# Kernel optimization log

Measured on AMD Instinct MI355X. Metric: run time of the kernel, lower is better.

Reference implementation:

```python
import jax, jax.numpy as jnp
import numpy as np

B, S, D_MODEL, H = 2, 2048, 512, 8
D_HEAD = D_MODEL // H  # 64; d_qk == d_model here


def setup_inputs() -> dict:
    key = jax.random.key(0)
    ks = jax.random.split(key, 7)
    sc = 1.0 / np.sqrt(D_MODEL)
    return {
        "x": jax.random.normal(ks[0], (B, S, D_MODEL), dtype=jnp.float32),
        "Wqk_w": jax.random.normal(ks[1], (2 * D_MODEL, D_MODEL), dtype=jnp.float32) * sc,
        "Wqk_b": jax.random.normal(ks[2], (2 * D_MODEL,), dtype=jnp.float32) * 0.01,
        "Wv_w": jax.random.normal(ks[3], (D_MODEL, D_MODEL), dtype=jnp.float32) * sc,
        "Wv_b": jax.random.normal(ks[4], (D_MODEL,), dtype=jnp.float32) * 0.01,
        "Wo_w": jax.random.normal(ks[5], (D_MODEL, D_MODEL), dtype=jnp.float32) * sc,
        "Wo_b": jax.random.normal(ks[6], (D_MODEL,), dtype=jnp.float32) * 0.01,
    }


def reference(x, Wqk_w, Wqk_b, Wv_w, Wv_b, Wo_w, Wo_b):
    b, s, _ = x.shape
    # projections
    qk = x @ Wqk_w.T + Wqk_b              # [B,S,2*d_qk]
    v = x @ Wv_w.T + Wv_b                 # [B,S,d_model]
    qk = qk.reshape(b, s, 2, H, D_HEAD)   # (two h d) layout
    v = v.reshape(b, s, H, D_HEAD)
    q, k = qk[:, :, 0], qk[:, :, 1]
    # generalized linear attention feature map: elu(x)+1
    q = jax.nn.elu(q) + 1.0
    k = jax.nn.elu(k) + 1.0
    scores = jnp.einsum('bthd,bshd->bhts', q, k)          # [B,H,T,S]
    mask = jnp.tril(jnp.ones((s, s), dtype=scores.dtype))  # causal multiplicative mask
    scores = scores * mask
    nu = scores.sum(axis=-1, keepdims=True)               # row normalizer
    attention = scores / nu
    context = jnp.einsum('bhts,bshd->bthd', attention, v)  # [B,T,H,D]
    out = context.reshape(b, s, D_MODEL) @ Wo_w.T + Wo_b
    return out
```

## Files before the change

kernel.cpp:

```cpp
#include <hip/hip_runtime.h>
#include <math.h>

#define B_N 2
#define S_N 2048
#define DM  512
#define H_N 8
#define DH  64
#define NC  32
#define CH  64

typedef __bf16 bf16x8 __attribute__((ext_vector_type(8)));
typedef float  f32x4  __attribute__((ext_vector_type(4)));

__device__ __forceinline__ unsigned short f2bf(float f) {
    unsigned int u = __float_as_uint(f);
    u += 0x7FFFu + ((u >> 16) & 1u);
    return (unsigned short)(u >> 16);
}
__device__ __forceinline__ float bf2f(unsigned short u) {
    return __uint_as_float((unsigned int)u << 16);
}

__device__ __forceinline__ void gload16(const void* g, void* l) {
    __builtin_amdgcn_global_load_lds(
        (const __attribute__((address_space(1))) unsigned int*)g,
        (__attribute__((address_space(3))) unsigned int*)l, 16, 0, 0);
}

__global__ __launch_bounds__(256) void convert_bf16(
    const float* __restrict__ x,  const float* __restrict__ wqk,
    const float* __restrict__ wv, const float* __restrict__ wo,
    unsigned short* __restrict__ xb,  unsigned short* __restrict__ wqkb,
    unsigned short* __restrict__ wvb, unsigned short* __restrict__ wob)
{
    int gid = blockIdx.x * 256 + threadIdx.x;
    const float* src; unsigned short* dst; int off;
    if (gid < 524288)      { src = x;   dst = xb;   off = gid; }
    else if (gid < 655360) { src = wqk; dst = wqkb; off = gid - 524288; }
    else if (gid < 720896) { src = wv;  dst = wvb;  off = gid - 655360; }
    else                   { src = wo;  dst = wob;  off = gid - 720896; }
    float4 v = ((const float4*)src)[off];
    ushort4 r; r.x = f2bf(v.x); r.y = f2bf(v.y); r.z = f2bf(v.z); r.w = f2bf(v.w);
    ((ushort4*)dst)[off] = r;
}

__global__ __launch_bounds__(256) void gemm_qkv_mfma(
    const unsigned short* __restrict__ xb,
    const unsigned short* __restrict__ Wqkb,
    const unsigned short* __restrict__ Wvb,
    const float* __restrict__ bqk, const float* __restrict__ bv,
    unsigned short* __restrict__ qb, unsigned short* __restrict__ kb_,
    unsigned short* __restrict__ ktb, unsigned short* __restrict__ vtb)
{
    __shared__ unsigned short Alds[128 * 32];
    __shared__ unsigned short Blds[128 * 32];
    const int tid = threadIdx.x;
    const int w = tid >> 6, l = tid & 63;
    const int wm = w >> 1, wn = w & 1;
    const int lane15 = l & 15, quad = l >> 4;
    const int n0 = blockIdx.x * 128;
    const int m0 = blockIdx.y * 128;

    const unsigned short* Wb; const float* bias; int nc0;
    if (n0 < 1024) { Wb = Wqkb; bias = bqk; nc0 = n0;        }
    else           { Wb = Wvb;  bias = bv;  nc0 = n0 - 1024; }

    const int srow = w * 16 + (l >> 2);
    const int skof = (l & 3) << 3;

    f32x4 acc[4][4];
    #pragma unroll
    for (int i = 0; i < 4; i++)
        #pragma unroll
        for (int j = 0; j < 4; j++) acc[i][j] = (f32x4){0.f, 0.f, 0.f, 0.f};

    for (int k0 = 0; k0 < DM; k0 += 32) {
        __syncthreads();
        gload16(&xb[(size_t)(m0 + srow) * DM + k0 + skof],       (char*)Alds + w * 1024);
        gload16(&xb[(size_t)(m0 + 64 + srow) * DM + k0 + skof],  (char*)Alds + 4096 + w * 1024);
        gload16(&Wb[(size_t)(nc0 + srow) * DM + k0 + skof],      (char*)Blds + w * 1024);
        gload16(&Wb[(size_t)(nc0 + 64 + srow) * DM + k0 + skof], (char*)Blds + 4096 + w * 1024);
        __syncthreads();

        bf16x8 af[4], bfr[4];
        #pragma unroll
        for (int i = 0; i < 4; i++) {
            af[i]  = *(bf16x8*)&Alds[(wm * 64 + i * 16 + lane15) * 32 + quad * 8];
            bfr[i] = *(bf16x8*)&Blds[(wn * 64 + i * 16 + lane15) * 32 + quad * 8];
        }
        #pragma unroll
        for (int i = 0; i < 4; i++)
            #pragma unroll
            for (int j = 0; j < 4; j++)
                acc[i][j] = __builtin_amdgcn_mfma_f32_16x16x32_bf16(af[i], bfr[j], acc[i][j], 0, 0, 0);
    }

    #pragma unroll
    for (int i = 0; i < 4; i++) {
        #pragma unroll
        for (int rg = 0; rg < 4; rg++) {
            int m = m0 + wm * 64 + i * 16 + quad * 4 + rg;
            int bb = m >> 11;
            int t  = m & (S_N - 1);
            #pragma unroll
            for (int j = 0; j < 4; j++) {
                int ncol = wn * 64 + j * 16 + lane15;
                float val = acc[i][j][rg] + bias[nc0 + ncol];
                int n = n0 + ncol;
                if (n < 1024) val = (val > 0.f) ? (val + 1.f) : __expf(val);
                unsigned short us = f2bf(val);
                if (n < 512) {
                    int h = n >> 6, d = n & 63;
                    qb[(((size_t)bb * H_N + h) * S_N + t) * DH + d] = us;
                } else if (n < 1024) {
                    int nn = n - 512, h = nn >> 6, d = nn & 63;
                    kb_[(((size_t)bb * H_N + h) * S_N + t) * DH + d] = us;
                    ktb[(((size_t)bb * H_N + h) * DH + d) * S_N + t] = us;
                } else {
                    int nn = n - 1024, h = nn >> 6, d = nn & 63;
                    vtb[(((size_t)bb * H_N + h) * DH + d) * S_N + t] = us;
                }
            }
        }
    }
}

__global__ __launch_bounds__(256) void chunk_sums_mfma(
    const unsigned short* __restrict__ ktb, const unsigned short* __restrict__ vtb,
    float* __restrict__ Asum, float* __restrict__ zsum)
{
    __shared__ float zpart[64][4];
    const int blk = blockIdx.x;
    const int bh = blk >> 5, c = blk & 31;
    const unsigned short* ktc = ktb + (size_t)bh * DH * S_N + c * CH;
    const unsigned short* vtc = vtb + (size_t)bh * DH * S_N + c * CH;
    const int tid = threadIdx.x;
    const int w = tid >> 6, l = tid & 63;
    const int lane15 = l & 15, quad = l >> 4;

    bf16x8 va[2];
    #pragma unroll
    for (int s = 0; s < 2; s++)
        va[s] = *(const bf16x8*)&vtc[(size_t)(w * 16 + lane15) * S_N + s * 32 + quad * 8];

    f32x4 acc[4];
    #pragma unroll
    for (int j = 0; j < 4; j++) acc[j] = (f32x4){0.f, 0.f, 0.f, 0.f};
    #pragma unroll
    for (int j = 0; j < 4; j++)
        #pragma unroll
        for (int s = 0; s < 2; s++) {
            bf16x8 kb = *(const bf16x8*)&ktc[(size_t)(j * 16 + lane15) * S_N + s * 32 + quad * 8];
            acc[j] = __builtin_amdgcn_mfma_f32_16x16x32_bf16(va[s], kb, acc[j], 0, 0, 0);
        }

    #pragma unroll
    for (int j = 0; j < 4; j++)
        #pragma unroll
        for (int rg = 0; rg < 4; rg++)
            Asum[(size_t)blk * 4096 + (w * 16 + quad * 4 + rg) * 64 + j * 16 + lane15] = acc[j][rg];

    const int d1 = tid >> 2, part = tid & 3;
    bf16x8 k0 = *(const bf16x8*)&ktc[(size_t)d1 * S_N + part * 16];
    bf16x8 k1 = *(const bf16x8*)&ktc[(size_t)d1 * S_N + part * 16 + 8];
    float zp = 0.f;
    #pragma unroll
    for (int i = 0; i < 8; i++) zp += (float)k0[i] + (float)k1[i];
    zpart[d1][part] = zp;
    __syncthreads();
    if (tid < 64)
        zsum[(size_t)blk * 64 + tid] = zpart[tid][0] + zpart[tid][1] + zpart[tid][2] + zpart[tid][3];
}

__global__ __launch_bounds__(256) void scan_states(
    const float* __restrict__ Asum, float* __restrict__ zsum,
    unsigned short* __restrict__ Sptb)
{
    const int gid = blockIdx.x * 256 + threadIdx.x;
    const int bh = gid / 4160;
    const int r  = gid % 4160;
    if (r < 4096) {
        size_t base = (size_t)bh * NC * 4096 + r;
        float acc = 0.f;
        for (int c = 0; c < NC; c++) {
            float tmp = Asum[base + (size_t)c * 4096];
            Sptb[base + (size_t)c * 4096] = f2bf(acc);
            acc += tmp;
        }
    } else {
        int d = r - 4096;
        size_t base = (size_t)bh * NC * 64 + d;
        float acc = 0.f;
        for (int c = 0; c < NC; c++) {
            float tmp = zsum[base + (size_t)c * 64];
            zsum[base + (size_t)c * 64] = acc;
            acc += tmp;
        }
    }
}

__global__ __launch_bounds__(256) void attn_mfma(
    const unsigned short* __restrict__ qb, const unsigned short* __restrict__ kb_,
    const unsigned short* __restrict__ vtb, const unsigned short* __restrict__ Sptb,
    const float* __restrict__ zsum, unsigned short* __restrict__ ctxb)
{
    __shared__ __align__(16) unsigned short P[64 * 72];
    __shared__ float nupart[64][4];

    const int blk = blockIdx.x;
    const int bh = blk >> 5, c = blk & 31;
    const int b = bh >> 3, h = bh & 7;
    const int tid = threadIdx.x;
    const int w = tid >> 6, l = tid & 63;
    const int lane15 = l & 15, quad = l >> 4;

    const unsigned short* qc  = qb  + (size_t)bh * S_N * DH + c * CH * DH;
    const unsigned short* kc  = kb_ + (size_t)bh * S_N * DH + c * CH * DH;
    const unsigned short* vtc = vtb + (size_t)bh * DH * S_N + c * CH;
    const unsigned short* spc = Sptb + (size_t)blk * 4096;
    const float* zc = zsum + (size_t)blk * 64;

    bf16x8 af[2];
    #pragma unroll
    for (int s = 0; s < 2; s++)
        af[s] = *(const bf16x8*)&qc[(w * 16 + lane15) * DH + s * 32 + quad * 8];

    f32x4 sacc[4];
    #pragma unroll
    for (int j = 0; j < 4; j++) sacc[j] = (f32x4){0.f, 0.f, 0.f, 0.f};
    #pragma unroll
    for (int j = 0; j < 4; j++)
        #pragma unroll
        for (int s = 0; s < 2; s++) {
            bf16x8 bk = *(const bf16x8*)&kc[(j * 16 + lane15) * DH + s * 32 + quad * 8];
            sacc[j] = __builtin_amdgcn_mfma_f32_16x16x32_bf16(af[s], bk, sacc[j], 0, 0, 0);
        }

    const int r0 = w * 16 + quad * 4;
    #pragma unroll
    for (int j = 0; j < 4; j++) {
        int u = j * 16 + lane15;
        #pragma unroll
        for (int rg = 0; rg < 4; rg++) {
            int rr = r0 + rg;
            float v = (u <= rr) ? sacc[j][rg] : 0.f;
            P[rr * 72 + u] = f2bf(v);
        }
    }
    __syncthreads();

    const int tl = tid >> 2, part = tid & 3;
    float nup = 0.f;
    {
        bf16x8 p0 = *(const bf16x8*)&P[tl * 72 + part * 16];
        bf16x8 p1 = *(const bf16x8*)&P[tl * 72 + part * 16 + 8];
        bf16x8 q0 = *(const bf16x8*)&qc[tl * DH + part * 16];
        bf16x8 q1 = *(const bf16x8*)&qc[tl * DH + part * 16 + 8];
        #pragma unroll
        for (int i = 0; i < 8; i++) {
            nup += (float)p0[i] + (float)p1[i];
            nup += (float)q0[i] * zc[part * 16 + i];
            nup += (float)q1[i] * zc[part * 16 + 8 + i];
        }
    }
    nupart[tl][part] = nup;
    __syncthreads();

    bf16x8 pa[2];
    #pragma unroll
    for (int s = 0; s < 2; s++)
        pa[s] = *(const bf16x8*)&P[(w * 16 + lane15) * 72 + s * 32 + quad * 8];

    f32x4 acc[4];
    #pragma unroll
    for (int j = 0; j < 4; j++) acc[j] = (f32x4){0.f, 0.f, 0.f, 0.f};
    #pragma unroll
    for (int j = 0; j < 4; j++)
        #pragma unroll
        for (int s = 0; s < 2; s++) {
            bf16x8 bv = *(const bf16x8*)&vtc[(size_t)(j * 16 + lane15) * S_N + s * 32 + quad * 8];
            acc[j] = __builtin_amdgcn_mfma_f32_16x16x32_bf16(pa[s], bv, acc[j], 0, 0, 0);
            bf16x8 bs = *(const bf16x8*)&spc[(j * 16 + lane15) * 64 + s * 32 + quad * 8];
            acc[j] = __builtin_amdgcn_mfma_f32_16x16x32_bf16(af[s], bs, acc[j], 0, 0, 0);
        }

    #pragma unroll
    for (int rg = 0; rg < 4; rg++) {
        int rr = r0 + rg;
        float nu = nupart[rr][0] + nupart[rr][1] + nupart[rr][2] + nupart[rr][3];
        float inv = 1.f / nu;
        size_t obase = ((size_t)b * S_N + c * CH + rr) * DM + h * DH;
        #pragma unroll
        for (int j = 0; j < 4; j++)
            ctxb[obase + j * 16 + lane15] = f2bf(acc[j][rg] * inv);
    }
}

__global__ __launch_bounds__(256) void gemm_out_mfma(
    const unsigned short* __restrict__ ctxb,
    const unsigned short* __restrict__ Wob,
    const float* __restrict__ bo, float* __restrict__ out)
{
    __shared__ unsigned short Alds[64 * 32];
    __shared__ unsigned short Blds[128 * 32];
    const int tid = threadIdx.x;
    const int w = tid >> 6, l = tid & 63;
    const int wm = w >> 1, wn = w & 1;
    const int lane15 = l & 15, quad = l >> 4;
    const int n0 = blockIdx.x * 128;
    const int m0 = blockIdx.y * 64;

    const int srow = w * 16 + (l >> 2);
    const int skof = (l & 3) << 3;

    f32x4 acc[2][4];
    #pragma unroll
    for (int i = 0; i < 2; i++)
        #pragma unroll
        for (int j = 0; j < 4; j++) acc[i][j] = (f32x4){0.f, 0.f, 0.f, 0.f};

    for (int k0 = 0; k0 < DM; k0 += 32) {
        __syncthreads();
        gload16(&ctxb[(size_t)(m0 + srow) * DM + k0 + skof],      (char*)Alds + w * 1024);
        gload16(&Wob[(size_t)(n0 + srow) * DM + k0 + skof],       (char*)Blds + w * 1024);
        gload16(&Wob[(size_t)(n0 + 64 + srow) * DM + k0 + skof],  (char*)Blds + 4096 + w * 1024);
        __syncthreads();

        bf16x8 af[2], bfr[4];
        #pragma unroll
        for (int i = 0; i < 2; i++)
            af[i] = *(bf16x8*)&Alds[(wm * 32 + i * 16 + lane15) * 32 + quad * 8];
        #pragma unroll
        for (int j = 0; j < 4; j++)
            bfr[j] = *(bf16x8*)&Blds[(wn * 64 + j * 16 + lane15) * 32 + quad * 8];
        #pragma unroll
        for (int i = 0; i < 2; i++)
            #pragma unroll
            for (int j = 0; j < 4; j++)
                acc[i][j] = __builtin_amdgcn_mfma_f32_16x16x32_bf16(af[i], bfr[j], acc[i][j], 0, 0, 0);
    }

    #pragma unroll
    for (int i = 0; i < 2; i++) {
        #pragma unroll
        for (int rg = 0; rg < 4; rg++) {
            int m = m0 + wm * 32 + i * 16 + quad * 4 + rg;
            #pragma unroll
            for (int j = 0; j < 4; j++) {
                int n = n0 + wn * 64 + j * 16 + lane15;
                out[(size_t)m * DM + n] = acc[i][j][rg] + bo[n];
            }
        }
    }
}

extern "C" void kernel_launch(void* const* d_in, const int* in_sizes, int n_in,
                              void* d_out, int out_size, void* d_ws, size_t ws_size,
                              hipStream_t stream)
{
    const float* x   = (const float*)d_in[0];
    const float* Wqk = (const float*)d_in[1];
    const float* bqk = (const float*)d_in[2];
    const float* Wv  = (const float*)d_in[3];
    const float* bv  = (const float*)d_in[4];
    const float* Wo  = (const float*)d_in[5];
    const float* bo  = (const float*)d_in[6];
    float* out = (float*)d_out;

    const size_t NTOK = (size_t)B_N * S_N * DM;
    float* Asum = (float*)d_ws;
    float* zsum = Asum + NTOK;
    unsigned short* xb   = (unsigned short*)(zsum + 32768);
    unsigned short* Wqkb = xb   + NTOK;
    unsigned short* Wvb  = Wqkb + 524288;
    unsigned short* Wob  = Wvb  + 262144;
    unsigned short* qb   = Wob  + 262144;
    unsigned short* kb_  = qb   + NTOK;
    unsigned short* ktb  = kb_  + NTOK;
    unsigned short* vtb  = ktb  + NTOK;
    unsigned short* Sptb = vtb  + NTOK;
    unsigned short* ctxb = Sptb + NTOK;

    convert_bf16   <<<dim3(3072),   256, 0, stream>>>(x, Wqk, Wv, Wo, xb, Wqkb, Wvb, Wob);
    gemm_qkv_mfma  <<<dim3(12, 32), 256, 0, stream>>>(xb, Wqkb, Wvb, bqk, bv, qb, kb_, ktb, vtb);
    chunk_sums_mfma<<<dim3(512),    256, 0, stream>>>(ktb, vtb, Asum, zsum);
    scan_states    <<<dim3(260),    256, 0, stream>>>(Asum, zsum, Sptb);
    attn_mfma      <<<dim3(512),    256, 0, stream>>>(qb, kb_, vtb, Sptb, zsum, ctxb);
    gemm_out_mfma  <<<dim3(4, 64),  256, 0, stream>>>(ctxb, Wob, bo, out);
}
```

Measured before the change: 130.1 us.

## Fuse per-chunk KV state sums into QKV projection GEMM epilogue

Reassigns the QKV GEMM tiles so that each non-Q block computes the K and V columns of a single head. The transposed K/V tiles are staged in shared memory. Each block then computes the per-chunk K^T V sums and the k-column sums directly, which removes the separate chunk_sums kernel. It also drops the transposed K global buffer, and V^T is written with coalesced vector stores from LDS instead of strided scalar stores. The cost is extra shared memory per block and a heavier epilogue that runs on only half of each block's waves.

```diff
diff --git a/kernel.cpp b/kernel.cpp
--- a/kernel.cpp
+++ b/kernel.cpp
@@ -16,9 +16,6 @@
     unsigned int u = __float_as_uint(f);
     u += 0x7FFFu + ((u >> 16) & 1u);
     return (unsigned short)(u >> 16);
-}
-__device__ __forceinline__ float bf2f(unsigned short u) {
-    return __uint_as_float((unsigned int)u << 16);
 }
 
 __device__ __forceinline__ void gload16(const void* g, void* l) {
@@ -44,26 +41,28 @@
     ((ushort4*)dst)[off] = r;
 }
 
-__global__ __launch_bounds__(256) void gemm_qkv_mfma(
+__global__ __launch_bounds__(256) void gemm_qkv_fused(
     const unsigned short* __restrict__ xb,
     const unsigned short* __restrict__ Wqkb,
     const unsigned short* __restrict__ Wvb,
     const float* __restrict__ bqk, const float* __restrict__ bv,
     unsigned short* __restrict__ qb, unsigned short* __restrict__ kb_,
-    unsigned short* __restrict__ ktb, unsigned short* __restrict__ vtb)
+    unsigned short* __restrict__ vtb,
+    float* __restrict__ Asum, float* __restrict__ zsum)
 {
     __shared__ unsigned short Alds[128 * 32];
     __shared__ unsigned short Blds[128 * 32];
+    __shared__ unsigned short ktT[64 * 136];
+    __shared__ unsigned short vtT[64 * 136];
+
     const int tid = threadIdx.x;
     const int w = tid >> 6, l = tid & 63;
     const int wm = w >> 1, wn = w & 1;
     const int lane15 = l & 15, quad = l >> 4;
-    const int n0 = blockIdx.x * 128;
+    const int bx = blockIdx.x;
     const int m0 = blockIdx.y * 128;
-
-    const unsigned short* Wb; const float* bias; int nc0;
-    if (n0 < 1024) { Wb = Wqkb; bias = bqk; nc0 = n0;        }
-    else           { Wb = Wvb;  bias = bv;  nc0 = n0 - 1024; }
+    const int isq = (bx < 4);
+    const int h = isq ? 0 : (bx - 4);
 
     const int srow = w * 16 + (l >> 2);
     const int skof = (l & 3) << 3;
@@ -76,10 +75,15 @@
 
     for (int k0 = 0; k0 < DM; k0 += 32) {
         __syncthreads();
-        gload16(&xb[(size_t)(m0 + srow) * DM + k0 + skof],       (char*)Alds + w * 1024);
-        gload16(&xb[(size_t)(m0 + 64 + srow) * DM + k0 + skof],  (char*)Alds + 4096 + w * 1024);
-        gload16(&Wb[(size_t)(nc0 + srow) * DM + k0 + skof],      (char*)Blds + w * 1024);
-        gload16(&Wb[(size_t)(nc0 + 64 + srow) * DM + k0 + skof], (char*)Blds + 4096 + w * 1024);
+        gload16(&xb[(size_t)(m0 + srow) * DM + k0 + skof],      (char*)Alds + w * 1024);
+        gload16(&xb[(size_t)(m0 + 64 + srow) * DM + k0 + skof], (char*)Alds + 4096 + w * 1024);
+        if (isq) {
+            gload16(&Wqkb[(size_t)(bx * 128 + srow) * DM + k0 + skof],      (char*)Blds + w * 1024);
+            gload16(&Wqkb[(size_t)(bx * 128 + 64 + srow) * DM + k0 + skof], (char*)Blds + 4096 + w * 1024);
+        } else {
+            gload16(&Wqkb[(size_t)(512 + h * 64 + srow) * DM + k0 + skof],  (char*)Blds + w * 1024);
+            gload16(&Wvb[(size_t)(h * 64 + srow) * DM + k0 + skof],         (char*)Blds + 4096 + w * 1024);
+        }
         __syncthreads();
 
         bf16x8 af[4], bfr[4];
@@ -95,81 +99,98 @@
                 acc[i][j] = __builtin_amdgcn_mfma_f32_16x16x32_bf16(af[i], bfr[j], acc[i][j], 0, 0, 0);
     }
 
-    #pragma unroll
-    for (int i = 0; i < 4; i++) {
-        #pragma unroll
-        for (int rg = 0; rg < 4; rg++) {
-            int m = m0 + wm * 64 + i * 16 + quad * 4 + rg;
-            int bb = m >> 11;
-            int t  = m & (S_N - 1);
-            #pragma unroll
-            for (int j = 0; j < 4; j++) {
-                int ncol = wn * 64 + j * 16 + lane15;
-                float val = acc[i][j][rg] + bias[nc0 + ncol];
-                int n = n0 + ncol;
-                if (n < 1024) val = (val > 0.f) ? (val + 1.f) : __expf(val);
-                unsigned short us = f2bf(val);
-                if (n < 512) {
-                    int h = n >> 6, d = n & 63;
-                    qb[(((size_t)bb * H_N + h) * S_N + t) * DH + d] = us;
-                } else if (n < 1024) {
-                    int nn = n - 512, h = nn >> 6, d = nn & 63;
-                    kb_[(((size_t)bb * H_N + h) * S_N + t) * DH + d] = us;
-                    ktb[(((size_t)bb * H_N + h) * DH + d) * S_N + t] = us;
-                } else {
-                    int nn = n - 1024, h = nn >> 6, d = nn & 63;
-                    vtb[(((size_t)bb * H_N + h) * DH + d) * S_N + t] = us;
+    const int bbu = m0 >> 11;
+    const int t0  = m0 & (S_N - 1);
+    const int c0  = t0 >> 6;
+
+    if (isq) {
+        #pragma unroll
+        for (int i = 0; i < 4; i++) {
+            #pragma unroll
+            for (int rg = 0; rg < 4; rg++) {
+                int m = m0 + wm * 64 + i * 16 + quad * 4 + rg;
+                int bb = m >> 11, t = m & (S_N - 1);
+                #pragma unroll
+                for (int j = 0; j < 4; j++) {
+                    int n = bx * 128 + wn * 64 + j * 16 + lane15;
+                    float val = acc[i][j][rg] + bqk[n];
+                    val = (val > 0.f) ? (val + 1.f) : __expf(val);
+                    qb[(((size_t)bb * H_N + (n >> 6)) * S_N + t) * DH + (n & 63)] = f2bf(val);
                 }
             }
         }
-    }
-}
-
-__global__ __launch_bounds__(256) void chunk_sums_mfma(
-    const unsigned short* __restrict__ ktb, const unsigned short* __restrict__ vtb,
-    float* __restrict__ Asum, float* __restrict__ zsum)
-{
-    __shared__ float zpart[64][4];
-    const int blk = blockIdx.x;
-    const int bh = blk >> 5, c = blk & 31;
-    const unsigned short* ktc = ktb + (size_t)bh * DH * S_N + c * CH;
-    const unsigned short* vtc = vtb + (size_t)bh * DH * S_N + c * CH;
-    const int tid = threadIdx.x;
-    const int w = tid >> 6, l = tid & 63;
-    const int lane15 = l & 15, quad = l >> 4;
-
-    bf16x8 va[2];
-    #pragma unroll
-    for (int s = 0; s < 2; s++)
-        va[s] = *(const bf16x8*)&vtc[(size_t)(w * 16 + lane15) * S_N + s * 32 + quad * 8];
-
-    f32x4 acc[4];
-    #pragma unroll
-    for (int j = 0; j < 4; j++) acc[j] = (f32x4){0.f, 0.f, 0.f, 0.f};
-    #pragma unroll
-    for (int j = 0; j < 4; j++)
-        #pragma unroll
-        for (int s = 0; s < 2; s++) {
-            bf16x8 kb = *(const bf16x8*)&ktc[(size_t)(j * 16 + lane15) * S_N + s * 32 + quad * 8];
-            acc[j] = __builtin_amdgcn_mfma_f32_16x16x32_bf16(va[s], kb, acc[j], 0, 0, 0);
-        }
-
-    #pragma unroll
-    for (int j = 0; j < 4; j++)
-        #pragma unroll
-        for (int rg = 0; rg < 4; rg++)
-            Asum[(size_t)blk * 4096 + (w * 16 + quad * 4 + rg) * 64 + j * 16 + lane15] = acc[j][rg];
-
-    const int d1 = tid >> 2, part = tid & 3;
-    bf16x8 k0 = *(const bf16x8*)&ktc[(size_t)d1 * S_N + part * 16];
-    bf16x8 k1 = *(const bf16x8*)&ktc[(size_t)d1 * S_N + part * 16 + 8];
-    float zp = 0.f;
-    #pragma unroll
-    for (int i = 0; i < 8; i++) zp += (float)k0[i] + (float)k1[i];
-    zpart[d1][part] = zp;
+        return;
+    }
+
+    #pragma unroll
+    for (int i = 0; i < 4; i++) {
+        #pragma unroll
+        for (int rg = 0; rg < 4; rg++) {
+            int tl = wm * 64 + i * 16 + quad * 4 + rg;
+            int t  = t0 + tl;
+            #pragma unroll
+            for (int j = 0; j < 4; j++) {
+                int col = j * 16 + lane15;
+                if (wn == 0) {
+                    float val = acc[i][j][rg] + bqk[512 + h * 64 + col];
+                    val = (val > 0.f) ? (val + 1.f) : __expf(val);
+                    unsigned short us = f2bf(val);
+                    kb_[(((size_t)bbu * H_N + h) * S_N + t) * DH + col] = us;
+                    ktT[col * 136 + tl] = us;
+                } else {
+                    float val = acc[i][j][rg] + bv[h * 64 + col];
+                    vtT[col * 136 + tl] = f2bf(val);
+                }
+            }
+        }
+    }
     __syncthreads();
-    if (tid < 64)
-        zsum[(size_t)blk * 64 + tid] = zpart[tid][0] + zpart[tid][1] + zpart[tid][2] + zpart[tid][3];
+
+    {
+        size_t vbase = (((size_t)bbu * H_N + h) * DH) * S_N + t0;
+        #pragma unroll
+        for (int it = 0; it < 4; it++) {
+            int idx = it * 2048 + tid * 8;
+            int d = idx >> 7, tt = idx & 127;
+            *(bf16x8*)&vtb[vbase + (size_t)d * S_N + tt] = *(bf16x8*)&vtT[d * 136 + tt];
+        }
+    }
+
+    #pragma unroll
+    for (int cc = 0; cc < 2; cc++) {
+        int blk = ((bbu * H_N + h) * NC) + c0 + cc;
+        bf16x8 va[2];
+        #pragma unroll
+        for (int s = 0; s < 2; s++)
+            va[s] = *(bf16x8*)&vtT[(w * 16 + lane15) * 136 + cc * 64 + s * 32 + quad * 8];
+        f32x4 sacc[4];
+        #pragma unroll
+        for (int j = 0; j < 4; j++) sacc[j] = (f32x4){0.f, 0.f, 0.f, 0.f};
+        #pragma unroll
+        for (int j = 0; j < 4; j++)
+            #pragma unroll
+            for (int s = 0; s < 2; s++) {
+                bf16x8 kB = *(bf16x8*)&ktT[(j * 16 + lane15) * 136 + cc * 64 + s * 32 + quad * 8];
+                sacc[j] = __builtin_amdgcn_mfma_f32_16x16x32_bf16(va[s], kB, sacc[j], 0, 0, 0);
+            }
+        #pragma unroll
+        for (int j = 0; j < 4; j++)
+            #pragma unroll
+            for (int rg = 0; rg < 4; rg++)
+                Asum[(size_t)blk * 4096 + (w * 16 + quad * 4 + rg) * 64 + j * 16 + lane15] = sacc[j][rg];
+    }
+
+    if (tid < 128) {
+        int cc = tid >> 6, d1 = tid & 63;
+        float z = 0.f;
+        #pragma unroll
+        for (int p = 0; p < 8; p++) {
+            bf16x8 kk = *(bf16x8*)&ktT[d1 * 136 + cc * 64 + p * 8];
+            #pragma unroll
+            for (int e = 0; e < 8; e++) z += (float)kk[e];
+        }
+        zsum[(size_t)((bbu * H_N + h) * NC + c0 + cc) * 64 + d1] = z;
+    }
 }
 
 __global__ __launch_bounds__(256) void scan_states(
@@ -376,15 +397,13 @@
     unsigned short* Wob  = Wvb  + 262144;
     unsigned short* qb   = Wob  + 262144;
     unsigned short* kb_  = qb   + NTOK;
-    unsigned short* ktb  = kb_  + NTOK;
-    unsigned short* vtb  = ktb  + NTOK;
+    unsigned short* vtb  = kb_  + NTOK;
     unsigned short* Sptb = vtb  + NTOK;
     unsigned short* ctxb = Sptb + NTOK;
 
-    convert_bf16   <<<dim3(3072),   256, 0, stream>>>(x, Wqk, Wv, Wo, xb, Wqkb, Wvb, Wob);
-    gemm_qkv_mfma  <<<dim3(12, 32), 256, 0, stream>>>(xb, Wqkb, Wvb, bqk, bv, qb, kb_, ktb, vtb);
-    chunk_sums_mfma<<<dim3(512),    256, 0, stream>>>(ktb, vtb, Asum, zsum);
-    scan_states    <<<dim3(260),    256, 0, stream>>>(Asum, zsum, Sptb);
-    attn_mfma      <<<dim3(512),    256, 0, stream>>>(qb, kb_, vtb, Sptb, zsum, ctxb);
-    gemm_out_mfma  <<<dim3(4, 64),  256, 0, stream>>>(ctxb, Wob, bo, out);
-}
+    convert_bf16  <<<dim3(3072),   256, 0, stream>>>(x, Wqk, Wv, Wo, xb, Wqkb, Wvb, Wob);
+    gemm_qkv_fused<<<dim3(12, 32), 256, 0, stream>>>(xb, Wqkb, Wvb, bqk, bv, qb, kb_, vtb, Asum, zsum);
+    scan_states   <<<dim3(260),    256, 0, stream>>>(Asum, zsum, Sptb);
+    attn_mfma     <<<dim3(512),    256, 0, stream>>>(qb, kb_, vtb, Sptb, zsum, ctxb);
+    gemm_out_mfma <<<dim3(4, 64),  256, 0, stream>>>(ctxb, Wob, bo, out);
+}
```

New measurement: 123.5 us. 5.1% less time.
